# Optimization experiments

Measured on AMD Instinct MI355X. Metric: run time of the kernel, lower is better.

The kernel has to match this reference:

```python
import jax, jax.numpy as jnp
import numpy as np
from jax import lax

B, T, F, C = 2, 249, 64, 256   # fixed by alpha/beta weight shapes in build()
K = 3                          # conv kernel size
FILT = 256                     # q/k conv filters (both blocks)
V = 256                        # v conv filters (both blocks)
OUT_CH = 64                    # conv2d_final filters (hardcoded)


def conv2d(x, w, b):
    # NHWC 'same' conv, stride 1, dilation 1
    return lax.conv_general_dilated(
        x, w, window_strides=(1, 1), padding='SAME',
        dimension_numbers=('NHWC', 'HWIO', 'NHWC')) + b


def attn_block(x, wq, bq, wk, bk, wv, bv):
    # x: [B, H, L, C]; attention over L per (batch, H) slice
    q = conv2d(x, wq, bq)          # [B,H,L,FILT]
    k = conv2d(x, wk, bk)          # [B,H,L,FILT]
    v = conv2d(x, wv, bv)          # [B,H,L,V]
    scores = jnp.einsum('bhqc,bhkc->bhqk', q, k)   # [B,H,L,L]
    dist = jax.nn.softmax(scores, axis=-1)
    return jnp.einsum('bhqk,bhkc->bhqc', dist, v)  # [B,H,L,V]


def setup_inputs() -> dict:
    key = jax.random.key(0)
    ks = jax.random.split(key, 18)
    s = 0.05
    d = {'x': jax.random.normal(ks[0], (B, T, F, C), jnp.float32)}
    names = ['wq_f', 'wk_f', 'wv_f', 'wq_t', 'wk_t', 'wv_t']
    outs = [FILT, FILT, V, FILT, FILT, V]
    for i, (n, o) in enumerate(zip(names, outs)):
        d[n] = jax.random.normal(ks[1 + i], (K, K, C, o), jnp.float32) * s
        d['b' + n[1:]] = jnp.zeros((o,), jnp.float32)
    d['w_final'] = jax.random.normal(ks[8], (K, K, V + V + C, OUT_CH), jnp.float32) * s
    d['b_final'] = jnp.zeros((OUT_CH,), jnp.float32)
    d['alpha'] = jax.random.uniform(ks[9], (B, T, F, V), jnp.float32, -0.05, 0.05)
    d['beta'] = jax.random.uniform(ks[10], (B, T, F, V), jnp.float32, -0.05, 0.05)
    return d


def reference(x, wq_f, bq_f, wk_f, bk_f, wv_f, bv_f,
              wq_t, bq_t, wk_t, bk_t, wv_t, bv_t,
              w_final, b_final, alpha, beta):
    # AFAB: transpose to [B,F,T,C], attend over time axis T
    xt = jnp.transpose(x, (0, 2, 1, 3))
    out_freq = attn_block(xt, wq_f, bq_f, wk_f, bk_f, wv_f, bv_f)
    out_freq = jnp.transpose(out_freq, (0, 2, 1, 3))  # back to [B,T,F,V]
    # ATAB: attend over frequency axis F directly on [B,T,F,C]
    out_time = attn_block(x, wq_t, bq_t, wk_t, bk_t, wv_t, bv_t)
    # learned elementwise gating + concat + final conv (concatenation=True path)
    fused = jnp.concatenate([alpha * out_freq, beta * out_time, x], axis=-1)
    return conv2d(fused, w_final, b_final)
```

## Files before the change

kernel.cpp:

```cpp
#include <hip/hip_runtime.h>


typedef _Float16 f16;
typedef _Float16 f16x8 __attribute__((ext_vector_type(8)));
typedef float    f32x4 __attribute__((ext_vector_type(4)));

#define B_   2
#define T_   249
#define F_   64
#define TP   251
#define FP   66
#define PIXB (T_*F_)
#define NPIX (B_*PIXB)
#define LPAD 256

static constexpr size_t FUSED_BYTES = (size_t)B_*TP*FP*768*2;
static constexpr size_t XPAD_BYTES  = (size_t)B_*TP*FP*256*2;
static constexpr size_t QF_BYTES    = (size_t)B_*64*LPAD*256*2;
static constexpr size_t QT_BYTES    = (size_t)B_*T_*64*256*2;
static constexpr size_t WT_BYTES    = (size_t)9*1536*256*2;
static constexpr size_t WFT_BYTES   = (size_t)9*64*768*2;

static constexpr size_t OFF_FUSED = 0;
static constexpr size_t OFF_XPAD  = OFF_FUSED + FUSED_BYTES;
static constexpr size_t OFF_QF    = OFF_XPAD  + XPAD_BYTES;
static constexpr size_t OFF_KF    = OFF_QF + QF_BYTES;
static constexpr size_t OFF_VF    = OFF_KF + QF_BYTES;
static constexpr size_t OFF_QT    = OFF_VF + QF_BYTES;
static constexpr size_t OFF_KT    = OFF_QT + QT_BYTES;
static constexpr size_t OFF_VT    = OFF_KT + QT_BYTES;
static constexpr size_t OFF_WT    = OFF_VT + QT_BYTES;
static constexpr size_t OFF_WFT   = OFF_WT + WT_BYTES;
static constexpr size_t OFF_BALL  = OFF_WFT + WFT_BYTES;
static constexpr size_t OFF_BF    = OFF_BALL + 1536*4;
static constexpr size_t WS_NEED   = OFF_BF + 64*4;

__device__ __forceinline__ f32x4 mfma16(f16x8 a, f16x8 b, f32x4 c) {
    return __builtin_amdgcn_mfma_f32_16x16x32_f16(a, b, c, 0, 0, 0);
}

__device__ __forceinline__ void gl_lds16(const void* g, void* l) {
    __builtin_amdgcn_global_load_lds(
        (const __attribute__((address_space(1))) unsigned int*)(unsigned long long)g,
        (__attribute__((address_space(3))) unsigned int*)(unsigned int)(unsigned long long)l,
        16, 0, 0);
}

__global__ __launch_bounds__(256) void prep_w(
    const float* __restrict__ wqf, const float* __restrict__ wkf, const float* __restrict__ wvf,
    const float* __restrict__ wqt, const float* __restrict__ wkt, const float* __restrict__ wvt,
    const float* __restrict__ wfin,
    const float* __restrict__ bqf, const float* __restrict__ bkf, const float* __restrict__ bvf,
    const float* __restrict__ bqt, const float* __restrict__ bkt, const float* __restrict__ bvt,
    const float* __restrict__ bfin,
    f16* __restrict__ wT, f16* __restrict__ wfT,
    float* __restrict__ biasAll, float* __restrict__ biasF)
{
    int idx = blockIdx.x*256 + threadIdx.x;
    if (idx < 9*1536*256) {
        int tap = idx / (1536*256);
        int r   = idx - tap*(1536*256);
        int n = r >> 8, c = r & 255;
        int dt = tap/3 - 1, df = tap%3 - 1;
        int blk = n >> 8, nl = n & 255;
        const float* w; int kh, kw;
        if (blk < 3) { w = (blk==0) ? wqf : (blk==1) ? wkf : wvf; kh = df+1; kw = dt+1; }
        else         { w = (blk==3) ? wqt : (blk==4) ? wkt : wvt; kh = dt+1; kw = df+1; }
        wT[idx] = (f16)w[((kh*3 + kw)*256 + c)*256 + nl];
    }
    if (idx < 9*64*768) {
        int tap = idx / (64*768);
        int r   = idx - tap*(64*768);
        int oc = r / 768, cin = r - oc*768;
        int dt = tap/3 - 1, df = tap%3 - 1;
        wfT[idx] = (f16)wfin[(((dt+1)*3 + (df+1))*768 + cin)*64 + oc];
    }
    if (idx < 1536) {
        int blk = idx >> 8, nl = idx & 255;
        const float* bb = (blk==0)?bqf:(blk==1)?bkf:(blk==2)?bvf:(blk==3)?bqt:(blk==4)?bkt:bvt;
        biasAll[idx] = bb[nl];
    }
    if (idx < 64) biasF[idx] = bfin[idx];
}

__global__ __launch_bounds__(256) void prep_x(
    const float* __restrict__ x, f16* __restrict__ xpad, f16* __restrict__ fused)
{
    int tid = blockIdx.x*256 + threadIdx.x;
    int pix = tid >> 5, c8 = (tid & 31)*8;
    int b = pix / PIXB; int r = pix - b*PIXB;
    int t = r >> 6, f = r & 63;
    const float* src = x + (size_t)pix*256 + c8;
    f16x8 v;
#pragma unroll
    for (int j = 0; j < 8; ++j) v[j] = (f16)src[j];
    size_t pp = (size_t)(b*TP + t + 1)*FP + (f + 1);
    *(f16x8*)(xpad + pp*256 + c8) = v;
    *(f16x8*)(fused + pp*768 + 512 + c8) = v;
}

__global__ __launch_bounds__(256) void border_zero(
    f16* __restrict__ xpad, f16* __restrict__ fused)
{
    int pix = blockIdx.x*2 + (threadIdx.x >> 7);
    int tl = threadIdx.x & 127;
    int b = pix / 630; int i = pix - b*630;
    int tp, fp;
    if (i < 66)       { tp = 0;   fp = i; }
    else if (i < 132) { tp = 250; fp = i - 66; }
    else { int j = i - 132; tp = 1 + (j >> 1); fp = (j & 1) * 65; }
    size_t pp = (size_t)(b*TP + tp)*FP + fp;
    f16x8 z = {0, 0, 0, 0, 0, 0, 0, 0};
    if (tl < 32) *(f16x8*)(xpad + pp*256 + tl*8) = z;
    if (tl < 96) *(f16x8*)(fused + pp*768 + tl*8) = z;
}

__global__ __launch_bounds__(256) void conv_qkv(
    const f16* __restrict__ xpad, const f16* __restrict__ wT,
    const float* __restrict__ biasAll,
    f16* __restrict__ qf, f16* __restrict__ kf, f16* __restrict__ vf,
    f16* __restrict__ qt, f16* __restrict__ kt_, f16* __restrict__ vt)
{
    __shared__ f16 smem[2][16384];
    const int l   = threadIdx.x & 63;
    const int wid = threadIdx.x >> 6;

    const int nwgq = 373, nwgr = 4;
    int xcd = blockIdx.x & 7, lin = blockIdx.x >> 3;
    int wg = (xcd < nwgr ? xcd*(nwgq+1) : nwgr*(nwgq+1) + (xcd-nwgr)*nwgq) + lin;
    const int mt = wg / 12;
    const int nt = wg - mt*12;
    const int wm = wid >> 1, wn = wid & 1;

    int aSrc[4], bSrc[4];
#pragma unroll
    for (int i = 0; i < 4; ++i) {
        int row = wid*32 + i*8 + (l >> 3);
        int ch  = (l & 7) ^ (row & 7);
        int p = mt*128 + row;
        int b = p / PIXB; int r = p - b*PIXB;
        int t = r >> 6, f = r & 63;
        aSrc[i] = ((b*TP + t + 1)*FP + (f + 1))*256 + ch*8;
        bSrc[i] = (nt*128 + row)*256 + ch*8;
    }

    int aRow[4], aSw[4], bRow[4], bSw[4];
#pragma unroll
    for (int mi = 0; mi < 4; ++mi) {
        int row = wm*64 + mi*16 + (l & 15);
        aRow[mi] = row*64; aSw[mi] = row & 7;
    }
#pragma unroll
    for (int ni = 0; ni < 4; ++ni) {
        int row = wn*64 + ni*16 + (l & 15);
        bRow[ni] = 8192 + row*64; bSw[ni] = row & 7;
    }

    f32x4 acc[4][4];
#pragma unroll
    for (int mi = 0; mi < 4; ++mi)
#pragma unroll
        for (int ni = 0; ni < 4; ++ni) acc[mi][ni] = {0.f, 0.f, 0.f, 0.f};

#define QSTAGE(KN, NB) do {                                                    \
        int tap_ = (KN) >> 2, kc_ = (KN) & 3;                                  \
        int ash_ = ((tap_/3 - 1)*FP + (tap_%3 - 1))*256 + kc_*64;              \
        const f16* wtap_ = wT + (size_t)tap_*(1536*256) + kc_*64;              \
        _Pragma("unroll")                                                      \
        for (int i_ = 0; i_ < 4; ++i_) {                                       \
            gl_lds16(xpad + aSrc[i_] + ash_, &smem[NB][(wid*32 + i_*8)*64]);   \
            gl_lds16(wtap_ + bSrc[i_], &smem[NB][8192 + (wid*32 + i_*8)*64]);  \
        }                                                                      \
    } while (0)

#define QCOMP(NB) do {                                                         \
        _Pragma("unroll")                                                      \
        for (int kk = 0; kk < 2; ++kk) {                                       \
            const int cch = kk*4 + (l >> 4);                                   \
            f16x8 af[4], bf[4];                                                \
            _Pragma("unroll")                                                  \
            for (int mi = 0; mi < 4; ++mi)                                     \
                af[mi] = *(const f16x8*)(&smem[NB][0] + aRow[mi] + ((cch ^ aSw[mi]) << 3)); \
            _Pragma("unroll")                                                  \
            for (int ni = 0; ni < 4; ++ni)                                     \
                bf[ni] = *(const f16x8*)(&smem[NB][0] + bRow[ni] + ((cch ^ bSw[ni]) << 3)); \
            __builtin_amdgcn_s_setprio(1);                                     \
            _Pragma("unroll")                                                  \
            for (int mi = 0; mi < 4; ++mi)                                     \
                _Pragma("unroll")                                              \
                for (int ni = 0; ni < 4; ++ni)                                 \
                    acc[mi][ni] = mfma16(af[mi], bf[ni], acc[mi][ni]);         \
            __builtin_amdgcn_s_setprio(0);                                     \
        }                                                                      \
    } while (0)

    QSTAGE(0, 0);
    __syncthreads();
    for (int kn = 0; kn < 36; kn += 2) {
        if (kn + 1 < 36) QSTAGE(kn + 1, 1);
        QCOMP(0);
        __syncthreads();
        if (kn + 2 < 36) QSTAGE(kn + 2, 0);
        QCOMP(1);
        __syncthreads();
    }
#undef QSTAGE
#undef QCOMP

    const int buf = nt >> 1;
    f16* dst = (buf==0)?qf:(buf==1)?kf:(buf==2)?vf:(buf==3)?qt:(buf==4)?kt_:vt;
#pragma unroll
    for (int mi = 0; mi < 4; ++mi) {
#pragma unroll
        for (int rg = 0; rg < 4; ++rg) {
            int row = wm*64 + mi*16 + (l >> 4)*4 + rg;
            int p = mt*128 + row;
            int b = p / PIXB; int r = p - b*PIXB;
            int t = r >> 6, f = r & 63;
#pragma unroll
            for (int ni = 0; ni < 4; ++ni) {
                int col = wn*64 + ni*16 + (l & 15);
                int ocg = nt*128 + col;
                int ocl = ocg & 255;
                float v = acc[mi][ni][rg] + biasAll[ocg];
                int off;
                if (buf < 2)       off = ((b*64 + f)*LPAD + t)*256 + ocl;
                else if (buf == 2) off = ((b*64 + f)*256 + ocl)*LPAD + t;
                else if (buf < 5)  off = ((b*T_ + t)*64 + f)*256 + ocl;
                else               off = ((b*T_ + t)*256 + ocl)*64 + f;
                dst[off] = (f16)v;
            }
        }
    }
}

__global__ __launch_bounds__(256) void attn_f(
    const f16* __restrict__ qf, const f16* __restrict__ kf, const f16* __restrict__ vf,
    const float* __restrict__ alpha, f16* __restrict__ fused)
{
    __shared__ f16 plds[4][16*256];
    const int l = threadIdx.x & 63;
    const int wid = threadIdx.x >> 6;
    const int head = blockIdx.x >> 2;
    const int qb = blockIdx.x & 3;
    const int b = head >> 6, f = head & 63;
    const f16* qh = qf + (size_t)head*LPAD*256;
    const f16* kh = kf + (size_t)head*LPAD*256;
    const f16* vh = vf + (size_t)head*256*LPAD;
    const int qr0 = qb*64 + wid*16;
    f16* pw = &plds[wid][0];

    f16x8 qa[8];
#pragma unroll
    for (int ks = 0; ks < 8; ++ks)
        qa[ks] = *(const f16x8*)(qh + (qr0 + (l & 15))*256 + ks*32 + (l >> 4)*8);

    f32x4 s[16];
#pragma unroll
    for (int nf = 0; nf < 16; ++nf) s[nf] = {0.f, 0.f, 0.f, 0.f};
#pragma unroll
    for (int ks = 0; ks < 8; ++ks)
#pragma unroll
        for (int nf = 0; nf < 16; ++nf) {
            f16x8 bf = *(const f16x8*)(kh + (nf*16 + (l & 15))*256 + ks*32 + (l >> 4)*8);
            s[nf] = mfma16(qa[ks], bf, s[nf]);
        }

    float inv[4];
#pragma unroll
    for (int rg = 0; rg < 4; ++rg) {
        float m = -1e30f;
#pragma unroll
        for (int nf = 0; nf < 16; ++nf)
            if (nf*16 + (l & 15) < T_) m = fmaxf(m, s[nf][rg]);
#pragma unroll
        for (int d = 1; d < 16; d <<= 1) m = fmaxf(m, __shfl_xor(m, d, 64));
        float sum = 0.f;
#pragma unroll
        for (int nf = 0; nf < 16; ++nf) {
            float p = (nf*16 + (l & 15) < T_) ? __expf(s[nf][rg] - m) : 0.f;
            s[nf][rg] = p;
            sum += p;
        }
#pragma unroll
        for (int d = 1; d < 16; d <<= 1) sum += __shfl_xor(sum, d, 64);
        inv[rg] = 1.f / sum;
    }

#pragma unroll
    for (int nf = 0; nf < 16; ++nf)
#pragma unroll
        for (int rg = 0; rg < 4; ++rg) {
            int row = (l >> 4)*4 + rg;
            int col = nf*16 + (l & 15);
            int byte = (row*512 + col*2) ^ ((row & 7) << 4);
            *(f16*)((char*)pw + byte) = (f16)s[nf][rg];
        }

    f32x4 o[16];
#pragma unroll
    for (int nf = 0; nf < 16; ++nf) o[nf] = {0.f, 0.f, 0.f, 0.f};
#pragma unroll
    for (int ks = 0; ks < 8; ++ks) {
        int row = l & 15;
        int cch = ks*4 + (l >> 4);
        int byte = row*512 + ((cch ^ (row & 7)) << 4);
        f16x8 pa = *(const f16x8*)((const char*)pw + byte);
#pragma unroll
        for (int nf = 0; nf < 16; ++nf) {
            f16x8 bf = *(const f16x8*)(vh + (nf*16 + (l & 15))*LPAD + ks*32 + (l >> 4)*8);
            o[nf] = mfma16(pa, bf, o[nf]);
        }
    }

#pragma unroll
    for (int rg = 0; rg < 4; ++rg) {
        int t = qr0 + (l >> 4)*4 + rg;
        if (t < T_) {
#pragma unroll
            for (int nf = 0; nf < 16; ++nf) {
                int c = nf*16 + (l & 15);
                float v = o[nf][rg] * inv[rg] * alpha[((size_t)(b*T_ + t)*64 + f)*256 + c];
                fused[((size_t)(b*TP + t + 1)*FP + (f + 1))*768 + c] = (f16)v;
            }
        }
    }
}

__global__ __launch_bounds__(256) void attn_t(
    const f16* __restrict__ qt, const f16* __restrict__ kt, const f16* __restrict__ vt,
    const float* __restrict__ beta, f16* __restrict__ fused)
{
    __shared__ f16 plds[4][16*64];
    const int l = threadIdx.x & 63;
    const int wid = threadIdx.x >> 6;
    const int head = blockIdx.x;
    const int b = head / T_, t = head - b*T_;
    const f16* qh = qt + (size_t)head*64*256;
    const f16* kh = kt + (size_t)head*64*256;
    const f16* vh = vt + (size_t)head*256*64;
    const int qr0 = wid*16;
    f16* pw = &plds[wid][0];

    f16x8 qa[8];
#pragma unroll
    for (int ks = 0; ks < 8; ++ks)
        qa[ks] = *(const f16x8*)(qh + (qr0 + (l & 15))*256 + ks*32 + (l >> 4)*8);

    f32x4 s[4];
#pragma unroll
    for (int nf = 0; nf < 4; ++nf) s[nf] = {0.f, 0.f, 0.f, 0.f};
#pragma unroll
    for (int ks = 0; ks < 8; ++ks)
#pragma unroll
        for (int nf = 0; nf < 4; ++nf) {
            f16x8 bf = *(const f16x8*)(kh + (nf*16 + (l & 15))*256 + ks*32 + (l >> 4)*8);
            s[nf] = mfma16(qa[ks], bf, s[nf]);
        }

    float inv[4];
#pragma unroll
    for (int rg = 0; rg < 4; ++rg) {
        float m = -1e30f;
#pragma unroll
        for (int nf = 0; nf < 4; ++nf) m = fmaxf(m, s[nf][rg]);
#pragma unroll
        for (int d = 1; d < 16; d <<= 1) m = fmaxf(m, __shfl_xor(m, d, 64));
        float sum = 0.f;
#pragma unroll
        for (int nf = 0; nf < 4; ++nf) {
            float p = __expf(s[nf][rg] - m);
            s[nf][rg] = p;
            sum += p;
        }
#pragma unroll
        for (int d = 1; d < 16; d <<= 1) sum += __shfl_xor(sum, d, 64);
        inv[rg] = 1.f / sum;
    }

#pragma unroll
    for (int nf = 0; nf < 4; ++nf)
#pragma unroll
        for (int rg = 0; rg < 4; ++rg) {
            int row = (l >> 4)*4 + rg;
            int col = nf*16 + (l & 15);
            int byte = (row*128 + col*2) ^ ((row & 7) << 4);
            *(f16*)((char*)pw + byte) = (f16)s[nf][rg];
        }

    f32x4 o[16];
#pragma unroll
    for (int nf = 0; nf < 16; ++nf) o[nf] = {0.f, 0.f, 0.f, 0.f};
#pragma unroll
    for (int ks = 0; ks < 2; ++ks) {
        int row = l & 15;
        int cch = ks*4 + (l >> 4);
        int byte = row*128 + ((cch ^ (row & 7)) << 4);
        f16x8 pa = *(const f16x8*)((const char*)pw + byte);
#pragma unroll
        for (int nf = 0; nf < 16; ++nf) {
            f16x8 bf = *(const f16x8*)(vh + (nf*16 + (l & 15))*64 + ks*32 + (l >> 4)*8);
            o[nf] = mfma16(pa, bf, o[nf]);
        }
    }

#pragma unroll
    for (int rg = 0; rg < 4; ++rg) {
        int fo = qr0 + (l >> 4)*4 + rg;
#pragma unroll
        for (int nf = 0; nf < 16; ++nf) {
            int c = nf*16 + (l & 15);
            float v = o[nf][rg] * inv[rg] * beta[((size_t)(b*T_ + t)*64 + fo)*256 + c];
            fused[((size_t)(b*TP + t + 1)*FP + (fo + 1))*768 + 256 + c] = (f16)v;
        }
    }
}

__global__ __launch_bounds__(256) void conv_final(
    const f16* __restrict__ fused, const f16* __restrict__ wfT,
    const float* __restrict__ biasF, float* __restrict__ out)
{
    __shared__ f16 smem[2][16384];
    const int l = threadIdx.x & 63;
    const int wid = threadIdx.x >> 6;
    const int mt = blockIdx.x;
    const int b = mt / T_, t = mt - b*T_;

    int aSrc[4], bSrc[4];
#pragma unroll
    for (int i = 0; i < 4; ++i) {
        int row = i*16 + wid*4 + (l >> 4);
        int ch  = (l & 15) ^ (row & 7);
        aSrc[i] = ((b*TP + t + 1)*FP + (row + 1))*768 + ch*8;
        bSrc[i] = row*768 + ch*8;
    }

    int aRowOff, aSwz;
    { int row = wid*16 + (l & 15); aRowOff = row*128; aSwz = row & 7; }
    int bRow[4], bSw[4];
#pragma unroll
    for (int ni = 0; ni < 4; ++ni) {
        int row = ni*16 + (l & 15);
        bRow[ni] = 8192 + row*128; bSw[ni] = row & 7;
    }

    f32x4 acc[4];
#pragma unroll
    for (int ni = 0; ni < 4; ++ni) acc[ni] = {0.f, 0.f, 0.f, 0.f};

#define FSTAGE(KN, NB) do {                                                    \
        int tap_ = (KN) / 6, kc_ = (KN) - ((KN)/6)*6;                          \
        int ash_ = ((tap_/3 - 1)*FP + (tap_%3 - 1))*768 + kc_*128;             \
        const f16* wt_ = wfT + (size_t)tap_*(64*768) + kc_*128;                \
        _Pragma("unroll")                                                      \
        for (int i_ = 0; i_ < 4; ++i_) {                                       \
            gl_lds16(fused + aSrc[i_] + ash_, &smem[NB][(i_*16 + wid*4)*128]); \
            gl_lds16(wt_ + bSrc[i_], &smem[NB][8192 + (i_*16 + wid*4)*128]);   \
        }                                                                      \
    } while (0)

#define FCOMP(NB) do {                                                         \
        _Pragma("unroll")                                                      \
        for (int kk = 0; kk < 4; ++kk) {                                       \
            const int cch = kk*4 + (l >> 4);                                   \
            f16x8 af = *(const f16x8*)(&smem[NB][0] + aRowOff + ((cch ^ aSwz) << 3)); \
            f16x8 bf[4];                                                       \
            _Pragma("unroll")                                                  \
            for (int ni = 0; ni < 4; ++ni)                                     \
                bf[ni] = *(const f16x8*)(&smem[NB][0] + bRow[ni] + ((cch ^ bSw[ni]) << 3)); \
            __builtin_amdgcn_s_setprio(1);                                     \
            _Pragma("unroll")                                                  \
            for (int ni = 0; ni < 4; ++ni)                                     \
                acc[ni] = mfma16(af, bf[ni], acc[ni]);                         \
            __builtin_amdgcn_s_setprio(0);                                     \
        }                                                                      \
    } while (0)

    FSTAGE(0, 0);
    __syncthreads();
    for (int kn = 0; kn < 54; kn += 2) {
        if (kn + 1 < 54) FSTAGE(kn + 1, 1);
        FCOMP(0);
        __syncthreads();
        if (kn + 2 < 54) FSTAGE(kn + 2, 0);
        FCOMP(1);
        __syncthreads();
    }
#undef FSTAGE
#undef FCOMP

#pragma unroll
    for (int rg = 0; rg < 4; ++rg) {
        int f = wid*16 + (l >> 4)*4 + rg;
        int p = mt*64 + f;
#pragma unroll
        for (int ni = 0; ni < 4; ++ni) {
            int oc = ni*16 + (l & 15);
            out[(size_t)p*64 + oc] = acc[ni][rg] + biasF[oc];
        }
    }
}

extern "C" void kernel_launch(void* const* d_in, const int* in_sizes, int n_in,
                              void* d_out, int out_size, void* d_ws, size_t ws_size,
                              hipStream_t stream) {
    (void)in_sizes; (void)n_in; (void)out_size;
    const float* x    = (const float*)d_in[0];
    const float* wqf  = (const float*)d_in[1];
    const float* bqf  = (const float*)d_in[2];
    const float* wkf  = (const float*)d_in[3];
    const float* bkf  = (const float*)d_in[4];
    const float* wvf  = (const float*)d_in[5];
    const float* bvf  = (const float*)d_in[6];
    const float* wqt  = (const float*)d_in[7];
    const float* bqt  = (const float*)d_in[8];
    const float* wkt  = (const float*)d_in[9];
    const float* bkt  = (const float*)d_in[10];
    const float* wvt  = (const float*)d_in[11];
    const float* bvt  = (const float*)d_in[12];
    const float* wfin = (const float*)d_in[13];
    const float* bfin = (const float*)d_in[14];
    const float* alpha= (const float*)d_in[15];
    const float* beta = (const float*)d_in[16];

    if (ws_size < WS_NEED) return;

    char* ws = (char*)d_ws;
    f16* fused  = (f16*)(ws + OFF_FUSED);
    f16* xpad   = (f16*)(ws + OFF_XPAD);
    f16* qf     = (f16*)(ws + OFF_QF);
    f16* kf     = (f16*)(ws + OFF_KF);
    f16* vf     = (f16*)(ws + OFF_VF);
    f16* qt     = (f16*)(ws + OFF_QT);
    f16* kt     = (f16*)(ws + OFF_KT);
    f16* vt     = (f16*)(ws + OFF_VT);
    f16* wT     = (f16*)(ws + OFF_WT);
    f16* wfT    = (f16*)(ws + OFF_WFT);
    float* bAll = (float*)(ws + OFF_BALL);
    float* bF   = (float*)(ws + OFF_BF);

    hipMemsetAsync(vf, 0, QF_BYTES, stream);

    border_zero<<<dim3(630), dim3(256), 0, stream>>>(xpad, fused);
    prep_w<<<dim3((9*1536*256 + 255)/256), dim3(256), 0, stream>>>(
        wqf, wkf, wvf, wqt, wkt, wvt, wfin,
        bqf, bkf, bvf, bqt, bkt, bvt, bfin, wT, wfT, bAll, bF);
    prep_x<<<dim3(NPIX*32/256), dim3(256), 0, stream>>>(x, xpad, fused);
    conv_qkv<<<dim3(2988), dim3(256), 0, stream>>>(xpad, wT, bAll, qf, kf, vf, qt, kt, vt);
    attn_f<<<dim3(512), dim3(256), 0, stream>>>(qf, kf, vf, alpha, fused);
    attn_t<<<dim3(498), dim3(256), 0, stream>>>(qt, kt, vt, beta, fused);
    conv_final<<<dim3(498), dim3(256), 0, stream>>>(fused, wfT, bF, (float*)d_out);
}
```

Measured before the change: 509.5 us.

## Enlarge conv_qkv tile to 256x128 with triple-buffered LDS pipeline

conv_qkv now runs 512-thread workgroups that each compute a 256-pixel by 128-channel tile, with eight waves sharing the weight tile. Staging moves from a double buffer with full __syncthreads to a three-stage LDS ring that uses partial vmcnt waits and raw barriers, so global-to-LDS loads can stay in flight across two compute stages. Tiles are mapped to XCDs so that each XCD works on a contiguous range of pixel tiles across all 12 channel tiles, and rows past the last pixel are clamped on load and skipped on store. The larger tile halves weight reloads per output, at the cost of more LDS (96KB) and lower occupancy.

```diff
diff --git a/kernel.cpp b/kernel.cpp
--- a/kernel.cpp
+++ b/kernel.cpp
@@ -115,62 +115,75 @@
     if (tl < 96) *(f16x8*)(fused + pp*768 + tl*8) = z;
 }
 
-__global__ __launch_bounds__(256) void conv_qkv(
+__global__ __launch_bounds__(512) void conv_qkv(
     const f16* __restrict__ xpad, const f16* __restrict__ wT,
     const float* __restrict__ biasAll,
     f16* __restrict__ qf, f16* __restrict__ kf, f16* __restrict__ vf,
     f16* __restrict__ qt, f16* __restrict__ kt_, f16* __restrict__ vt)
 {
-    __shared__ f16 smem[2][16384];
+    __shared__ f16 smem[3*24576];
+
+    const int xcd = blockIdx.x & 7, lin = blockIdx.x >> 3;
+    const int mtcnt  = (xcd < 5) ? 16 : 15;
+    if (lin >= 12*mtcnt) return;
+    const int mtbase = (xcd < 5) ? xcd*16 : 80 + (xcd - 5)*15;
+    int nt, mi;
+    if (xcd < 5) { nt = lin >> 4; mi = lin & 15; }
+    else         { nt = lin / 15; mi = lin - nt*15; }
+    const int mt = mtbase + mi;
+
     const int l   = threadIdx.x & 63;
     const int wid = threadIdx.x >> 6;
-
-    const int nwgq = 373, nwgr = 4;
-    int xcd = blockIdx.x & 7, lin = blockIdx.x >> 3;
-    int wg = (xcd < nwgr ? xcd*(nwgq+1) : nwgr*(nwgq+1) + (xcd-nwgr)*nwgq) + lin;
-    const int mt = wg / 12;
-    const int nt = wg - mt*12;
     const int wm = wid >> 1, wn = wid & 1;
 
-    int aSrc[4], bSrc[4];
+    int aSrc[4], bSrc[2];
 #pragma unroll
     for (int i = 0; i < 4; ++i) {
-        int row = wid*32 + i*8 + (l >> 3);
+        int row = i*64 + wid*8 + (l >> 3);
         int ch  = (l & 7) ^ (row & 7);
-        int p = mt*128 + row;
+        int p = mt*256 + row;
+        if (p > NPIX - 1) p = NPIX - 1;
         int b = p / PIXB; int r = p - b*PIXB;
         int t = r >> 6, f = r & 63;
         aSrc[i] = ((b*TP + t + 1)*FP + (f + 1))*256 + ch*8;
-        bSrc[i] = (nt*128 + row)*256 + ch*8;
+    }
+#pragma unroll
+    for (int j = 0; j < 2; ++j) {
+        int row = j*64 + wid*8 + (l >> 3);
+        int ch  = (l & 7) ^ (row & 7);
+        bSrc[j] = (nt*128 + row)*256 + ch*8;
     }
 
     int aRow[4], aSw[4], bRow[4], bSw[4];
 #pragma unroll
-    for (int mi = 0; mi < 4; ++mi) {
-        int row = wm*64 + mi*16 + (l & 15);
-        aRow[mi] = row*64; aSw[mi] = row & 7;
+    for (int mi2 = 0; mi2 < 4; ++mi2) {
+        int row = wm*64 + mi2*16 + (l & 15);
+        aRow[mi2] = row*64; aSw[mi2] = row & 7;
     }
 #pragma unroll
     for (int ni = 0; ni < 4; ++ni) {
         int row = wn*64 + ni*16 + (l & 15);
-        bRow[ni] = 8192 + row*64; bSw[ni] = row & 7;
+        bRow[ni] = 16384 + row*64; bSw[ni] = row & 7;
     }
 
     f32x4 acc[4][4];
 #pragma unroll
-    for (int mi = 0; mi < 4; ++mi)
-#pragma unroll
-        for (int ni = 0; ni < 4; ++ni) acc[mi][ni] = {0.f, 0.f, 0.f, 0.f};
+    for (int mi2 = 0; mi2 < 4; ++mi2)
+#pragma unroll
+        for (int ni = 0; ni < 4; ++ni) acc[mi2][ni] = {0.f, 0.f, 0.f, 0.f};
 
 #define QSTAGE(KN, NB) do {                                                    \
         int tap_ = (KN) >> 2, kc_ = (KN) & 3;                                  \
         int ash_ = ((tap_/3 - 1)*FP + (tap_%3 - 1))*256 + kc_*64;              \
         const f16* wtap_ = wT + (size_t)tap_*(1536*256) + kc_*64;              \
         _Pragma("unroll")                                                      \
-        for (int i_ = 0; i_ < 4; ++i_) {                                       \
-            gl_lds16(xpad + aSrc[i_] + ash_, &smem[NB][(wid*32 + i_*8)*64]);   \
-            gl_lds16(wtap_ + bSrc[i_], &smem[NB][8192 + (wid*32 + i_*8)*64]);  \
-        }                                                                      \
+        for (int i_ = 0; i_ < 4; ++i_)                                         \
+            gl_lds16(xpad + aSrc[i_] + ash_,                                   \
+                     &smem[(NB)*24576 + (i_*64 + wid*8)*64]);                  \
+        _Pragma("unroll")                                                      \
+        for (int j_ = 0; j_ < 2; ++j_)                                         \
+            gl_lds16(wtap_ + bSrc[j_],                                         \
+                     &smem[(NB)*24576 + 16384 + (j_*64 + wid*8)*64]);          \
     } while (0)
 
 #define QCOMP(NB) do {                                                         \
@@ -179,42 +192,53 @@
             const int cch = kk*4 + (l >> 4);                                   \
             f16x8 af[4], bf[4];                                                \
             _Pragma("unroll")                                                  \
-            for (int mi = 0; mi < 4; ++mi)                                     \
-                af[mi] = *(const f16x8*)(&smem[NB][0] + aRow[mi] + ((cch ^ aSw[mi]) << 3)); \
+            for (int mi2 = 0; mi2 < 4; ++mi2)                                  \
+                af[mi2] = *(const f16x8*)(&smem[(NB)*24576] + aRow[mi2] + ((cch ^ aSw[mi2]) << 3)); \
             _Pragma("unroll")                                                  \
             for (int ni = 0; ni < 4; ++ni)                                     \
-                bf[ni] = *(const f16x8*)(&smem[NB][0] + bRow[ni] + ((cch ^ bSw[ni]) << 3)); \
+                bf[ni] = *(const f16x8*)(&smem[(NB)*24576] + bRow[ni] + ((cch ^ bSw[ni]) << 3)); \
             __builtin_amdgcn_s_setprio(1);                                     \
             _Pragma("unroll")                                                  \
-            for (int mi = 0; mi < 4; ++mi)                                     \
+            for (int mi2 = 0; mi2 < 4; ++mi2)                                  \
                 _Pragma("unroll")                                              \
                 for (int ni = 0; ni < 4; ++ni)                                 \
-                    acc[mi][ni] = mfma16(af[mi], bf[ni], acc[mi][ni]);         \
+                    acc[mi2][ni] = mfma16(af[mi2], bf[ni], acc[mi2][ni]);      \
             __builtin_amdgcn_s_setprio(0);                                     \
         }                                                                      \
     } while (0)
 
+#define VM6  asm volatile("s_waitcnt vmcnt(6)" ::: "memory")
+#define VM0  asm volatile("s_waitcnt vmcnt(0)" ::: "memory")
+#define BAR  __builtin_amdgcn_s_barrier()
+
     QSTAGE(0, 0);
-    __syncthreads();
-    for (int kn = 0; kn < 36; kn += 2) {
-        if (kn + 1 < 36) QSTAGE(kn + 1, 1);
-        QCOMP(0);
-        __syncthreads();
-        if (kn + 2 < 36) QSTAGE(kn + 2, 0);
-        QCOMP(1);
-        __syncthreads();
-    }
+    QSTAGE(1, 1);
+    VM6; BAR;
+#pragma unroll 1
+    for (int m = 0; m < 11; ++m) {
+        const int kn = m*3;
+        QSTAGE(kn + 2, 2); QCOMP(0); VM6; BAR;
+        QSTAGE(kn + 3, 0); QCOMP(1); VM6; BAR;
+        QSTAGE(kn + 4, 1); QCOMP(2); VM6; BAR;
+    }
+    QSTAGE(35, 2); QCOMP(0); VM6; BAR;
+    QCOMP(1);               VM0; BAR;
+    QCOMP(2);
 #undef QSTAGE
 #undef QCOMP
+#undef VM6
+#undef VM0
+#undef BAR
 
     const int buf = nt >> 1;
     f16* dst = (buf==0)?qf:(buf==1)?kf:(buf==2)?vf:(buf==3)?qt:(buf==4)?kt_:vt;
 #pragma unroll
-    for (int mi = 0; mi < 4; ++mi) {
+    for (int mi2 = 0; mi2 < 4; ++mi2) {
 #pragma unroll
         for (int rg = 0; rg < 4; ++rg) {
-            int row = wm*64 + mi*16 + (l >> 4)*4 + rg;
-            int p = mt*128 + row;
+            int row = wm*64 + mi2*16 + (l >> 4)*4 + rg;
+            int p = mt*256 + row;
+            if (p >= NPIX) continue;
             int b = p / PIXB; int r = p - b*PIXB;
             int t = r >> 6, f = r & 63;
 #pragma unroll
@@ -222,7 +246,7 @@
                 int col = wn*64 + ni*16 + (l & 15);
                 int ocg = nt*128 + col;
                 int ocl = ocg & 255;
-                float v = acc[mi][ni][rg] + biasAll[ocg];
+                float v = acc[mi2][ni][rg] + biasAll[ocg];
                 int off;
                 if (buf < 2)       off = ((b*64 + f)*LPAD + t)*256 + ocl;
                 else if (buf == 2) off = ((b*64 + f)*256 + ocl)*LPAD + t;
@@ -546,7 +570,7 @@
         wqf, wkf, wvf, wqt, wkt, wvt, wfin,
         bqf, bkf, bvf, bqt, bkt, bvt, bfin, wT, wfT, bAll, bF);
     prep_x<<<dim3(NPIX*32/256), dim3(256), 0, stream>>>(x, xpad, fused);
-    conv_qkv<<<dim3(2988), dim3(256), 0, stream>>>(xpad, wT, bAll, qf, kf, vf, qt, kt, vt);
+    conv_qkv<<<dim3(1536), dim3(512), 0, stream>>>(xpad, wT, bAll, qf, kf, vf, qt, kt, vt);
     attn_f<<<dim3(512), dim3(256), 0, stream>>>(qf, kf, vf, alpha, fused);
     attn_t<<<dim3(498), dim3(256), 0, stream>>>(qt, kt, vt, beta, fused);
     conv_final<<<dim3(498), dim3(256), 0, stream>>>(fused, wfT, bF, (float*)d_out);
```

New measurement: 508.8 us. About the same (-0.1%).

## Restructure QKV conv to load input halo once per channel chunk and reuse across taps

Applied to the files above, without the earlier changes.

The QKV implicit-GEMM conv now stages a halo tile of input rows (4 time rows plus padding) into shared memory once per 64-channel chunk, and reuses it across all nine taps by offsetting positions. Previously the input was reloaded from global memory for every tap. Tiles grow to 256x256 with 512 threads and an 8x4 accumulator per wave, and only the weight tiles are double-buffered. Blocks are remapped per XCD so neighbouring M tiles share L2. The cost is higher register pressure from 32 accumulators, a larger LDS footprint, idle early-exit blocks, and wasted rows in the last time tile.

```diff
diff --git a/kernel.cpp b/kernel.cpp
--- a/kernel.cpp
+++ b/kernel.cpp
@@ -13,6 +13,7 @@
 #define PIXB (T_*F_)
 #define NPIX (B_*PIXB)
 #define LPAD 256
+#define XPOS (B_*TP*FP)
 
 static constexpr size_t FUSED_BYTES = (size_t)B_*TP*FP*768*2;
 static constexpr size_t XPAD_BYTES  = (size_t)B_*TP*FP*256*2;
@@ -115,120 +116,148 @@
     if (tl < 96) *(f16x8*)(fused + pp*768 + tl*8) = z;
 }
 
-__global__ __launch_bounds__(256) void conv_qkv(
+__global__ __launch_bounds__(512, 2) void conv_qkv(
     const f16* __restrict__ xpad, const f16* __restrict__ wT,
     const float* __restrict__ biasAll,
     f16* __restrict__ qf, f16* __restrict__ kf, f16* __restrict__ vf,
     f16* __restrict__ qt, f16* __restrict__ kt_, f16* __restrict__ vt)
 {
-    __shared__ f16 smem[2][16384];
+    __shared__ f16 smemH[448*64];
+    __shared__ f16 smemB[2][256*64];
+
+    const int xcd = blockIdx.x & 7, lin = blockIdx.x >> 3;
+    const int mtcnt = (xcd < 6) ? 16 : 15;
+    if (lin >= 6*mtcnt) return;
+    const int mtbase = (xcd < 6) ? xcd*16 : 96 + (xcd - 6)*15;
+    const int nt = lin / mtcnt;
+    const int mt = mtbase + (lin - nt*mtcnt);
+
+    const int bb_ = mt / 63;
+    const int t0  = (mt - bb_*63) * 4;
+    const int Gs66 = (bb_*TP + t0) * 66;
+
     const int l   = threadIdx.x & 63;
     const int wid = threadIdx.x >> 6;
-
-    const int nwgq = 373, nwgr = 4;
-    int xcd = blockIdx.x & 7, lin = blockIdx.x >> 3;
-    int wg = (xcd < nwgr ? xcd*(nwgq+1) : nwgr*(nwgq+1) + (xcd-nwgr)*nwgq) + lin;
-    const int mt = wg / 12;
-    const int nt = wg - mt*12;
-    const int wm = wid >> 1, wn = wid & 1;
-
-    int aSrc[4], bSrc[4];
-#pragma unroll
-    for (int i = 0; i < 4; ++i) {
-        int row = wid*32 + i*8 + (l >> 3);
-        int ch  = (l & 7) ^ (row & 7);
-        int p = mt*128 + row;
-        int b = p / PIXB; int r = p - b*PIXB;
-        int t = r >> 6, f = r & 63;
-        aSrc[i] = ((b*TP + t + 1)*FP + (f + 1))*256 + ch*8;
-        bSrc[i] = (nt*128 + row)*256 + ch*8;
-    }
-
-    int aRow[4], aSw[4], bRow[4], bSw[4];
-#pragma unroll
-    for (int mi = 0; mi < 4; ++mi) {
-        int row = wm*64 + mi*16 + (l & 15);
-        aRow[mi] = row*64; aSw[mi] = row & 7;
-    }
-#pragma unroll
-    for (int ni = 0; ni < 4; ++ni) {
-        int row = wn*64 + ni*16 + (l & 15);
-        bRow[ni] = 8192 + row*64; bSw[ni] = row & 7;
-    }
-
-    f32x4 acc[4][4];
-#pragma unroll
-    for (int mi = 0; mi < 4; ++mi)
-#pragma unroll
-        for (int ni = 0; ni < 4; ++ni) acc[mi][ni] = {0.f, 0.f, 0.f, 0.f};
-
-#define QSTAGE(KN, NB) do {                                                    \
-        int tap_ = (KN) >> 2, kc_ = (KN) & 3;                                  \
-        int ash_ = ((tap_/3 - 1)*FP + (tap_%3 - 1))*256 + kc_*64;              \
-        const f16* wtap_ = wT + (size_t)tap_*(1536*256) + kc_*64;              \
+    const int wm = wid >> 2, wn = wid & 3;
+
+    int hOff[7];
+#pragma unroll
+    for (int j = 0; j < 7; ++j) {
+        int pos = j*64 + wid*8 + (l >> 3);
+        int ps = pos;
+        if (ps > 395) ps = 395;
+        int pmax = (XPOS - 1) - Gs66/1;
+        { int pm = XPOS - 1 - (bb_*TP + t0)*66; if (ps > pm) ps = pm; }
+        (void)pmax;
+        int ch = (l & 7) ^ (ps & 7);
+        hOff[j] = (Gs66 + ps)*256 + ch*8;
+    }
+    int bSrc[4];
+#pragma unroll
+    for (int j = 0; j < 4; ++j) {
+        int row = j*64 + wid*8 + (l >> 3);
+        int ch = (l & 7) ^ (row & 7);
+        bSrc[j] = (nt*256 + row)*256 + ch*8;
+    }
+
+    int pos00[8];
+#pragma unroll
+    for (int m = 0; m < 8; ++m) {
+        int r = wm*128 + m*16 + (l & 15);
+        pos00[m] = ((r >> 6) + 1)*66 + (r & 63) + 1;
+    }
+    int bRow[4], bSw[4];
+#pragma unroll
+    for (int n = 0; n < 4; ++n) {
+        int row = wn*64 + n*16 + (l & 15);
+        bRow[n] = row*64; bSw[n] = row & 7;
+    }
+
+    f32x4 acc[8][4];
+#pragma unroll
+    for (int m = 0; m < 8; ++m)
+#pragma unroll
+        for (int n = 0; n < 4; ++n) acc[m][n] = {0.f, 0.f, 0.f, 0.f};
+
+#define HSTAGE(C) do {                                                         \
         _Pragma("unroll")                                                      \
-        for (int i_ = 0; i_ < 4; ++i_) {                                       \
-            gl_lds16(xpad + aSrc[i_] + ash_, &smem[NB][(wid*32 + i_*8)*64]);   \
-            gl_lds16(wtap_ + bSrc[i_], &smem[NB][8192 + (wid*32 + i_*8)*64]);  \
-        }                                                                      \
+        for (int j_ = 0; j_ < 7; ++j_)                                         \
+            gl_lds16(xpad + hOff[j_] + (C)*64,                                 \
+                     smemH + (j_*512 + wid*64)*8);                             \
     } while (0)
 
-#define QCOMP(NB) do {                                                         \
+#define BSTAGE(TAP, C, NB) do {                                                \
+        const f16* wt_ = wT + (size_t)(TAP)*(1536*256) + (C)*64;               \
+        _Pragma("unroll")                                                      \
+        for (int j_ = 0; j_ < 4; ++j_)                                         \
+            gl_lds16(wt_ + bSrc[j_], &smemB[NB][(j_*512 + wid*64)*8]);         \
+    } while (0)
+
+#define QCOMP(NB, TAPOFF) do {                                                 \
+        int pos_[8];                                                           \
+        _Pragma("unroll")                                                      \
+        for (int m = 0; m < 8; ++m) pos_[m] = pos00[m] + (TAPOFF);             \
         _Pragma("unroll")                                                      \
         for (int kk = 0; kk < 2; ++kk) {                                       \
             const int cch = kk*4 + (l >> 4);                                   \
-            f16x8 af[4], bf[4];                                                \
+            f16x8 af[8], bf[4];                                                \
             _Pragma("unroll")                                                  \
-            for (int mi = 0; mi < 4; ++mi)                                     \
-                af[mi] = *(const f16x8*)(&smem[NB][0] + aRow[mi] + ((cch ^ aSw[mi]) << 3)); \
+            for (int m = 0; m < 8; ++m)                                        \
+                af[m] = *(const f16x8*)(smemH + pos_[m]*64 + ((cch ^ (pos_[m] & 7)) << 3)); \
             _Pragma("unroll")                                                  \
-            for (int ni = 0; ni < 4; ++ni)                                     \
-                bf[ni] = *(const f16x8*)(&smem[NB][0] + bRow[ni] + ((cch ^ bSw[ni]) << 3)); \
+            for (int n = 0; n < 4; ++n)                                        \
+                bf[n] = *(const f16x8*)(&smemB[NB][0] + bRow[n] + ((cch ^ bSw[n]) << 3)); \
             __builtin_amdgcn_s_setprio(1);                                     \
             _Pragma("unroll")                                                  \
-            for (int mi = 0; mi < 4; ++mi)                                     \
+            for (int m = 0; m < 8; ++m)                                        \
                 _Pragma("unroll")                                              \
-                for (int ni = 0; ni < 4; ++ni)                                 \
-                    acc[mi][ni] = mfma16(af[mi], bf[ni], acc[mi][ni]);         \
+                for (int n = 0; n < 4; ++n)                                    \
+                    acc[m][n] = mfma16(af[m], bf[n], acc[m][n]);               \
             __builtin_amdgcn_s_setprio(0);                                     \
         }                                                                      \
     } while (0)
 
-    QSTAGE(0, 0);
+    int buf = 0;
+    HSTAGE(0);
+    BSTAGE(0, 0, 0);
     __syncthreads();
-    for (int kn = 0; kn < 36; kn += 2) {
-        if (kn + 1 < 36) QSTAGE(kn + 1, 1);
-        QCOMP(0);
-        __syncthreads();
-        if (kn + 2 < 36) QSTAGE(kn + 2, 0);
-        QCOMP(1);
-        __syncthreads();
-    }
-#undef QSTAGE
+    for (int c = 0; c < 4; ++c) {
+        for (int tap = 0; tap < 9; ++tap) {
+            if (tap < 8)      BSTAGE(tap + 1, c, buf ^ 1);
+            else if (c < 3)   BSTAGE(0, c + 1, buf ^ 1);
+            const int dt = tap/3 - 1, df = tap - (tap/3)*3 - 1;
+            QCOMP(buf, dt*66 + df);
+            __syncthreads();
+            buf ^= 1;
+        }
+        if (c < 3) {
+            HSTAGE(c + 1);
+            __syncthreads();
+        }
+    }
+#undef HSTAGE
+#undef BSTAGE
 #undef QCOMP
 
-    const int buf = nt >> 1;
-    f16* dst = (buf==0)?qf:(buf==1)?kf:(buf==2)?vf:(buf==3)?qt:(buf==4)?kt_:vt;
-#pragma unroll
-    for (int mi = 0; mi < 4; ++mi) {
+    f16* dst = (nt==0)?qf:(nt==1)?kf:(nt==2)?vf:(nt==3)?qt:(nt==4)?kt_:vt;
+#pragma unroll
+    for (int m = 0; m < 8; ++m) {
 #pragma unroll
         for (int rg = 0; rg < 4; ++rg) {
-            int row = wm*64 + mi*16 + (l >> 4)*4 + rg;
-            int p = mt*128 + row;
-            int b = p / PIXB; int r = p - b*PIXB;
-            int t = r >> 6, f = r & 63;
-#pragma unroll
-            for (int ni = 0; ni < 4; ++ni) {
-                int col = wn*64 + ni*16 + (l & 15);
-                int ocg = nt*128 + col;
-                int ocl = ocg & 255;
-                float v = acc[mi][ni][rg] + biasAll[ocg];
-                int off;
-                if (buf < 2)       off = ((b*64 + f)*LPAD + t)*256 + ocl;
-                else if (buf == 2) off = ((b*64 + f)*256 + ocl)*LPAD + t;
-                else if (buf < 5)  off = ((b*T_ + t)*64 + f)*256 + ocl;
-                else               off = ((b*T_ + t)*256 + ocl)*64 + f;
-                dst[off] = (f16)v;
+            int row = wm*128 + m*16 + (l >> 4)*4 + rg;
+            int t = t0 + (row >> 6), f = row & 63;
+            if (t <= 248) {
+#pragma unroll
+                for (int n = 0; n < 4; ++n) {
+                    int col = wn*64 + n*16 + (l & 15);
+                    float v = acc[m][n][rg] + biasAll[nt*256 + col];
+                    int off;
+                    if (nt < 2)       off = ((bb_*64 + f)*LPAD + t)*256 + col;
+                    else if (nt == 2) off = ((bb_*64 + f)*256 + col)*LPAD + t;
+                    else if (nt < 5)  off = ((bb_*T_ + t)*64 + f)*256 + col;
+                    else              off = ((bb_*T_ + t)*256 + col)*64 + f;
+                    dst[off] = (f16)v;
+                }
             }
         }
     }
@@ -546,7 +575,7 @@
         wqf, wkf, wvf, wqt, wkt, wvt, wfin,
         bqf, bkf, bvf, bqt, bkt, bvt, bfin, wT, wfT, bAll, bF);
     prep_x<<<dim3(NPIX*32/256), dim3(256), 0, stream>>>(x, xpad, fused);
-    conv_qkv<<<dim3(2988), dim3(256), 0, stream>>>(xpad, wT, bAll, qf, kf, vf, qt, kt, vt);
+    conv_qkv<<<dim3(768), dim3(512), 0, stream>>>(xpad, wT, bAll, qf, kf, vf, qt, kt, vt);
     attn_f<<<dim3(512), dim3(256), 0, stream>>>(qf, kf, vf, alpha, fused);
     attn_t<<<dim3(498), dim3(256), 0, stream>>>(qt, kt, vt, beta, fused);
     conv_final<<<dim3(498), dim3(256), 0, stream>>>(fused, wfT, bF, (float*)d_out);
```

After: 496.2 us. 2.6% less time.
